# Optimization experiments

Measured on AMD Instinct MI355X. Metric: run time of the kernel, lower is better.

## Reference

```python
import jax, jax.numpy as jnp
import numpy as np

MUL0, MUL1, MUL2, NMOD = 128, 64, 32, 2  # multiplicities of 0e,1e,2e and modalities
D0, D1, D2 = MUL0, MUL1 * 3, MUL2 * 5     # 128, 192, 160 -> total 480


def setup_inputs() -> dict:
    key = jax.random.key(0)
    ks = jax.random.split(key, 7)
    N, G = 200000, 512
    x = jax.random.normal(ks[0], (N, D0 + D1 + D2), dtype=jnp.float32)
    modal_attr = jax.random.uniform(ks[1], (G, NMOD), dtype=jnp.float32)
    W0 = jax.random.normal(ks[2], (MUL0, MUL0), dtype=jnp.float32)
    W0m = jax.random.normal(ks[3], (NMOD, MUL0), dtype=jnp.float32)
    W1 = jax.random.normal(ks[4], (MUL1, MUL1), dtype=jnp.float32)
    W2 = jax.random.normal(ks[5], (MUL2, MUL2), dtype=jnp.float32)
    batch = jnp.sort(jax.random.randint(ks[6], (N,), 0, G, dtype=jnp.int64))
    return {"x": x, "modal_attr": modal_attr, "W0": W0, "W0m": W0m,
            "W1": W1, "W2": W2, "batch": batch}


def reference(x, modal_attr, W0, W0m, W1, W2, batch):
    N = x.shape[0]
    # modality one-hot gathered per node and concatenated (appended 2x0e irrep)
    modal = modal_attr[batch]  # [N, NMOD]
    x0 = x[:, :D0]                                   # [N, 128]  0e
    x1 = x[:, D0:D0 + D1].reshape(N, MUL1, 3)        # [N, 64, 3] 1e
    x2 = x[:, D0 + D1:].reshape(N, MUL2, 5)          # [N, 32, 5] 2e
    # e3nn Linear: per-(l,p) block linear, paths summed, /sqrt(total fan-in mul)
    inv0 = 1.0 / np.sqrt(MUL0 + NMOD).astype(np.float32)
    out0 = (x0 @ W0 + modal @ W0m) * inv0            # [N, 128]
    out1 = jnp.einsum('nim,io->nom', x1, W1) * (1.0 / np.sqrt(MUL1).astype(np.float32))
    out2 = jnp.einsum('nim,io->nom', x2, W2) * (1.0 / np.sqrt(MUL2).astype(np.float32))
    return jnp.concatenate([out0, out1.reshape(N, D1), out2.reshape(N, D2)], axis=1)
```

## Files before the change

### kernel.cpp

```cpp
#include <hip/hip_runtime.h>
#include <hip/hip_bf16.h>


typedef __attribute__((ext_vector_type(8))) short  short8;
typedef __attribute__((ext_vector_type(4))) float  f32x4;

#define NTH 256
#define BR  32

#define W0H 0
#define W0L 16384
#define W1H 32768
#define W1L 36864
#define W2H 40960
#define W2L 41984

#define IN0   0
#define OUT0  24576

__device__ __forceinline__ unsigned bc2(__hip_bfloat162 h) {
    unsigned u; __builtin_memcpy(&u, &h, 4); return u;
}

struct HL4 { uint2 h, l; };

__device__ __forceinline__ HL4 split4(float a, float b, float c, float d) {
    __hip_bfloat162 h01 = __float22bfloat162_rn({a, b});
    __hip_bfloat162 h23 = __float22bfloat162_rn({c, d});
    float ra = a - __low2float(h01),  rb = b - __high2float(h01);
    float rc = c - __low2float(h23),  rd = d - __high2float(h23);
    __hip_bfloat162 l01 = __float22bfloat162_rn({ra, rb});
    __hip_bfloat162 l23 = __float22bfloat162_rn({rc, rd});
    HL4 r;
    r.h = make_uint2(bc2(h01), bc2(h23));
    r.l = make_uint2(bc2(l01), bc2(l23));
    return r;
}

__device__ __forceinline__ void split_w(float v, unsigned short& h, unsigned short& l) {
    __hip_bfloat16 hb = __float2bfloat16(v);
    float r = v - __bfloat162float(hb);
    __hip_bfloat16 lb = __float2bfloat16(r);
    __builtin_memcpy(&h, &hb, 2);
    __builtin_memcpy(&l, &lb, 2);
}

__global__ void prep_weights(const float* __restrict__ W0,
                             const float* __restrict__ W1,
                             const float* __restrict__ W2,
                             unsigned short* __restrict__ ws) {
    const int s0     = blockIdx.x * blockDim.x + threadIdx.x;
    const int STRIDE = gridDim.x * blockDim.x;
    for (int s = s0; s < 16384; s += STRIDE) {
        int j = s & 7, l = (s >> 3) & 63, kt = (s >> 9) & 3, ct = s >> 11;
        int col = ct * 16 + (l & 15);
        int k   = kt * 32 + (l >> 4) * 8 + j;
        unsigned short h, lo;
        split_w(W0[k * 128 + col], h, lo);
        ws[W0H + s] = h; ws[W0L + s] = lo;
    }
    for (int s = s0; s < 4096; s += STRIDE) {
        int j = s & 7, l = (s >> 3) & 63, kt = (s >> 9) & 1, ct = s >> 10;
        int col = ct * 16 + (l & 15);
        int k   = kt * 32 + (l >> 4) * 8 + j;
        unsigned short h, lo;
        split_w(W1[k * 64 + col], h, lo);
        ws[W1H + s] = h; ws[W1L + s] = lo;
    }
    for (int s = s0; s < 1024; s += STRIDE) {
        int j = s & 7, l = (s >> 3) & 63, ct = s >> 9;
        int col = ct * 16 + (l & 15);
        int k   = (l >> 4) * 8 + j;
        unsigned short h, lo;
        split_w(W2[k * 32 + col], h, lo);
        ws[W2H + s] = h; ws[W2L + s] = lo;
    }
}

#define MFMA(a, b, c) __builtin_amdgcn_mfma_f32_16x16x32_bf16((a), (b), (c), 0, 0, 0)

__global__ __launch_bounds__(NTH, 3) void irreps_mfma_kernel(
    const float* __restrict__ x,
    const float* __restrict__ modal_attr,
    const float* __restrict__ W0m,
    const unsigned short* __restrict__ wsf,
    const int*   __restrict__ batch,
    float*       __restrict__ out,
    int N)
{
    __shared__ __align__(16) char ldsb[49664];
    char*  inb  = ldsb + IN0;
    float* ldsf = reinterpret_cast<float*>(ldsb + OUT0);

    const int tid  = threadIdx.x;
    const int w    = tid >> 6;
    const int l    = tid & 63;
    const int r    = l & 15;
    const int kg   = l >> 4;
    const int rb0  = (w >> 1) * 16;
    const int ch   = w & 1;
    const int row0 = blockIdx.x * BR;
    const int arow = rb0 + r;

    float am0[4], am1[4];
    #pragma unroll
    for (int reg = 0; reg < 4; ++reg) {
        int n  = row0 + rb0 + kg * 4 + reg;
        int nc = n < N ? n : N - 1;
        int g  = batch[nc];
        am0[reg] = modal_attr[2 * g];
        am1[reg] = modal_attr[2 * g + 1];
    }

    const float4* __restrict__ x4 = reinterpret_cast<const float4*>(x);

    {
        const int seg = tid & 15;
        const int rr0 = tid >> 4;
        #pragma unroll
        for (int t2 = 0; t2 < 2; ++t2) {
            int rr = rr0 + 16 * t2;
            int n  = row0 + rr; n = n < N ? n : N - 1;
            const float4* src = &x4[(size_t)n * 120 + seg * 2];
            float4 a = src[0], b = src[1];
            HL4 p = split4(a.x, a.y, a.z, a.w);
            HL4 q = split4(b.x, b.y, b.z, b.w);
            int byte = (rr * 256 + seg * 16) ^ ((rr & 7) << 4);
            *reinterpret_cast<uint4*>(inb + byte)        = make_uint4(p.h.x, p.h.y, q.h.x, q.h.y);
            *reinterpret_cast<uint4*>(inb + 8192 + byte) = make_uint4(p.l.x, p.l.y, q.l.x, q.l.y);
        }
    }

    float4 bld[2][3];
    {
        const int ig  = tid & 15;
        const int rr0 = tid >> 4;
        #pragma unroll
        for (int t2 = 0; t2 < 2; ++t2) {
            int rr = rr0 + 16 * t2;
            int n  = row0 + rr; n = n < N ? n : N - 1;
            const float4* src = &x4[(size_t)n * 120 + 32 + ig * 3];
            bld[t2][0] = src[0]; bld[t2][1] = src[1]; bld[t2][2] = src[2];
        }
    }
    __syncthreads();

    {
        const int sw = (arow & 7) << 4;
        short8 ah[4], al[4];
        #pragma unroll
        for (int kt = 0; kt < 4; ++kt) {
            int byte = (arow * 256 + kt * 64 + kg * 16) ^ sw;
            ah[kt] = *reinterpret_cast<const short8*>(inb + byte);
            al[kt] = *reinterpret_cast<const short8*>(inb + 8192 + byte);
        }
        #pragma unroll
        for (int ci = 0; ci < 4; ++ci) {
            int ct = ch * 4 + ci;
            f32x4 acc = {0.f, 0.f, 0.f, 0.f};
            #pragma unroll
            for (int kt = 0; kt < 4; ++kt) {
                int b = ct * 4 + kt;
                short8 bh = *reinterpret_cast<const short8*>(wsf + W0H + (size_t)(b * 64 + l) * 8);
                short8 bl = *reinterpret_cast<const short8*>(wsf + W0L + (size_t)(b * 64 + l) * 8);
                acc = MFMA(ah[kt], bh, acc);
                acc = MFMA(al[kt], bh, acc);
                acc = MFMA(ah[kt], bl, acc);
            }
            int col = ct * 16 + r;
            float wm0 = W0m[col], wm1 = W0m[128 + col];
            #pragma unroll
            for (int reg = 0; reg < 4; ++reg)
                ldsf[(rb0 + kg * 4 + reg) * 132 + col] =
                    (acc[reg] + am0[reg] * wm0 + am1[reg] * wm1) * 0.08770580193070293f;
        }
    }
    __syncthreads();

    {
        const int ig  = tid & 15;
        const int rr0 = tid >> 4;
        #pragma unroll
        for (int t2 = 0; t2 < 2; ++t2) {
            int rr = rr0 + 16 * t2;
            float4 f0 = bld[t2][0], f1 = bld[t2][1], f2 = bld[t2][2];
            HL4 s0 = split4(f0.x, f0.w, f1.z, f2.y);
            HL4 s1 = split4(f0.y, f1.x, f1.w, f2.z);
            HL4 s2 = split4(f0.z, f1.y, f2.x, f2.w);
            int rbyte = (rr * 128 + ig * 8) ^ ((rr & 7) << 4);
            *reinterpret_cast<uint2*>(inb + 0 * 4096 + rbyte)         = s0.h;
            *reinterpret_cast<uint2*>(inb + 1 * 4096 + rbyte)         = s1.h;
            *reinterpret_cast<uint2*>(inb + 2 * 4096 + rbyte)         = s2.h;
            *reinterpret_cast<uint2*>(inb + 12288 + 0 * 4096 + rbyte) = s0.l;
            *reinterpret_cast<uint2*>(inb + 12288 + 1 * 4096 + rbyte) = s1.l;
            *reinterpret_cast<uint2*>(inb + 12288 + 2 * 4096 + rbyte) = s2.l;
        }
    }
    float4 cld[5];
    {
        int rr = tid >> 3, ig = tid & 7;
        int n  = row0 + rr; n = n < N ? n : N - 1;
        const float4* src = &x4[(size_t)n * 120 + 80 + ig * 5];
        #pragma unroll
        for (int q = 0; q < 5; ++q) cld[q] = src[q];
    }
    {
        #pragma unroll
        for (int j = 0; j < 4; ++j) {
            int idx = tid + j * NTH;
            int row = idx >> 5, c4 = idx & 31;
            int n   = row0 + row;
            if (n < N)
                *reinterpret_cast<float4*>(out + (size_t)n * 480 + c4 * 4) =
                    *reinterpret_cast<const float4*>(ldsf + row * 132 + c4 * 4);
        }
    }
    __syncthreads();

    {
        const int sw = (arow & 7) << 4;
        short8 ah1[3][2], al1[3][2];
        #pragma unroll
        for (int m = 0; m < 3; ++m) {
            #pragma unroll
            for (int kt = 0; kt < 2; ++kt) {
                int byte = (arow * 128 + kt * 64 + kg * 16) ^ sw;
                ah1[m][kt] = *reinterpret_cast<const short8*>(inb + m * 4096 + byte);
                al1[m][kt] = *reinterpret_cast<const short8*>(inb + 12288 + m * 4096 + byte);
            }
        }
        #pragma unroll
        for (int ci = 0; ci < 2; ++ci) {
            int ct = ch * 2 + ci;
            short8 bh[2], bl[2];
            #pragma unroll
            for (int kt = 0; kt < 2; ++kt) {
                int b = ct * 2 + kt;
                bh[kt] = *reinterpret_cast<const short8*>(wsf + W1H + (size_t)(b * 64 + l) * 8);
                bl[kt] = *reinterpret_cast<const short8*>(wsf + W1L + (size_t)(b * 64 + l) * 8);
            }
            #pragma unroll
            for (int m = 0; m < 3; ++m) {
                f32x4 acc = {0.f, 0.f, 0.f, 0.f};
                #pragma unroll
                for (int kt = 0; kt < 2; ++kt) {
                    acc = MFMA(ah1[m][kt], bh[kt], acc);
                    acc = MFMA(al1[m][kt], bh[kt], acc);
                    acc = MFMA(ah1[m][kt], bl[kt], acc);
                }
                int col = 3 * (ct * 16 + r) + m;
                #pragma unroll
                for (int reg = 0; reg < 4; ++reg)
                    ldsf[(rb0 + kg * 4 + reg) * 196 + col] = acc[reg] * 0.125f;
            }
        }
    }
    __syncthreads();

    {
        int rr = tid >> 3, ig = tid & 7;
        float f[20];
        #pragma unroll
        for (int q = 0; q < 5; ++q) {
            float4 v = cld[q];
            f[q * 4 + 0] = v.x; f[q * 4 + 1] = v.y; f[q * 4 + 2] = v.z; f[q * 4 + 3] = v.w;
        }
        int rbyte = (rr * 64 + ig * 8) ^ ((rr & 3) << 4);
        #pragma unroll
        for (int m = 0; m < 5; ++m) {
            HL4 s = split4(f[m], f[5 + m], f[10 + m], f[15 + m]);
            *reinterpret_cast<uint2*>(inb + m * 2048 + rbyte)         = s.h;
            *reinterpret_cast<uint2*>(inb + 10240 + m * 2048 + rbyte) = s.l;
        }
    }
    {
        #pragma unroll
        for (int j = 0; j < 6; ++j) {
            int idx = tid + j * NTH;
            int row = idx / 48, c4 = idx - row * 48;
            int n   = row0 + row;
            if (n < N)
                *reinterpret_cast<float4*>(out + (size_t)n * 480 + 128 + c4 * 4) =
                    *reinterpret_cast<const float4*>(ldsf + row * 196 + c4 * 4);
        }
    }
    __syncthreads();

    {
        const int sw2 = (arow & 3) << 4;
        short8 ah2[5], al2[5];
        #pragma unroll
        for (int m = 0; m < 5; ++m) {
            int byte = (arow * 64 + kg * 16) ^ sw2;
            ah2[m] = *reinterpret_cast<const short8*>(inb + m * 2048 + byte);
            al2[m] = *reinterpret_cast<const short8*>(inb + 10240 + m * 2048 + byte);
        }
        int ct = ch;
        short8 bh = *reinterpret_cast<const short8*>(wsf + W2H + (size_t)(ct * 64 + l) * 8);
        short8 bl = *reinterpret_cast<const short8*>(wsf + W2L + (size_t)(ct * 64 + l) * 8);
        #pragma unroll
        for (int m = 0; m < 5; ++m) {
            f32x4 acc = {0.f, 0.f, 0.f, 0.f};
            acc = MFMA(ah2[m], bh, acc);
            acc = MFMA(al2[m], bh, acc);
            acc = MFMA(ah2[m], bl, acc);
            int col = 5 * (ct * 16 + r) + m;
            #pragma unroll
            for (int reg = 0; reg < 4; ++reg)
                ldsf[(rb0 + kg * 4 + reg) * 164 + col] = acc[reg] * 0.17677669529663687f;
        }
    }
    __syncthreads();

    {
        #pragma unroll
        for (int j = 0; j < 5; ++j) {
            int idx = tid + j * NTH;
            int row = idx / 40, c4 = idx - row * 40;
            int n   = row0 + row;
            if (n < N)
                *reinterpret_cast<float4*>(out + (size_t)n * 480 + 320 + c4 * 4) =
                    *reinterpret_cast<const float4*>(ldsf + row * 164 + c4 * 4);
        }
    }
}

extern "C" void kernel_launch(void* const* d_in, const int* in_sizes, int n_in,
                              void* d_out, int out_size, void* d_ws, size_t ws_size,
                              hipStream_t stream) {
    const float* x     = (const float*)d_in[0];
    const float* modal = (const float*)d_in[1];
    const float* W0    = (const float*)d_in[2];
    const float* W0m   = (const float*)d_in[3];
    const float* W1    = (const float*)d_in[4];
    const float* W2    = (const float*)d_in[5];
    const int*   batch = (const int*)d_in[6];
    float* out = (float*)d_out;
    unsigned short* ws = (unsigned short*)d_ws;

    const int N    = in_sizes[6];
    const int grid = (N + BR - 1) / BR;

    prep_weights<<<84, NTH, 0, stream>>>(W0, W1, W2, ws);
    irreps_mfma_kernel<<<grid, NTH, 0, stream>>>(x, modal, W0m, ws, batch, out, N);
}
```

Before: 159.5 us.

## Swap MFMA operands to write outputs directly from registers, dropping LDS staging

MFMA operands are swapped so the weights become the A operand and node rows the B operand. Each lane then holds four consecutive output columns for a single row and can write float4 directly to global memory, with no round-trip through an LDS output buffer. This drops the output staging region, cuts LDS to 24 KB and raises the launch-bounds occupancy target from 3 to 4. The stores are now per-row float4 writes spread over 16 rows per wave, which may coalesce less well than the previous contiguous row copies. The modal lookup is also reduced to one row per lane.

```diff
diff --git a/kernel.cpp b/kernel.cpp
--- a/kernel.cpp
+++ b/kernel.cpp
@@ -14,9 +14,6 @@
 #define W1L 36864
 #define W2H 40960
 #define W2L 41984
-
-#define IN0   0
-#define OUT0  24576
 
 __device__ __forceinline__ unsigned bc2(__hip_bfloat162 h) {
     unsigned u; __builtin_memcpy(&u, &h, 4); return u;
@@ -79,7 +76,7 @@
 
 #define MFMA(a, b, c) __builtin_amdgcn_mfma_f32_16x16x32_bf16((a), (b), (c), 0, 0, 0)
 
-__global__ __launch_bounds__(NTH, 3) void irreps_mfma_kernel(
+__global__ __launch_bounds__(NTH, 4) void irreps_mfma_kernel(
     const float* __restrict__ x,
     const float* __restrict__ modal_attr,
     const float* __restrict__ W0m,
@@ -88,9 +85,7 @@
     float*       __restrict__ out,
     int N)
 {
-    __shared__ __align__(16) char ldsb[49664];
-    char*  inb  = ldsb + IN0;
-    float* ldsf = reinterpret_cast<float*>(ldsb + OUT0);
+    __shared__ __align__(16) char inb[24576];
 
     const int tid  = threadIdx.x;
     const int w    = tid >> 6;
@@ -102,15 +97,13 @@
     const int row0 = blockIdx.x * BR;
     const int arow = rb0 + r;
 
-    float am0[4], am1[4];
-    #pragma unroll
-    for (int reg = 0; reg < 4; ++reg) {
-        int n  = row0 + rb0 + kg * 4 + reg;
-        int nc = n < N ? n : N - 1;
-        int g  = batch[nc];
-        am0[reg] = modal_attr[2 * g];
-        am1[reg] = modal_attr[2 * g + 1];
-    }
+    const int  n_mine = row0 + arow;
+    const bool ok     = n_mine < N;
+    const int  nc     = ok ? n_mine : N - 1;
+    const int  g      = batch[nc];
+    const float m0 = modal_attr[2 * g];
+    const float m1 = modal_attr[2 * g + 1];
+    float* __restrict__ orow = out + (size_t)n_mine * 480;
 
     const float4* __restrict__ x4 = reinterpret_cast<const float4*>(x);
 
@@ -145,34 +138,14 @@
     }
     __syncthreads();
 
+    short8 xh[4], xl[4];
     {
         const int sw = (arow & 7) << 4;
-        short8 ah[4], al[4];
         #pragma unroll
         for (int kt = 0; kt < 4; ++kt) {
             int byte = (arow * 256 + kt * 64 + kg * 16) ^ sw;
-            ah[kt] = *reinterpret_cast<const short8*>(inb + byte);
-            al[kt] = *reinterpret_cast<const short8*>(inb + 8192 + byte);
-        }
-        #pragma unroll
-        for (int ci = 0; ci < 4; ++ci) {
-            int ct = ch * 4 + ci;
-            f32x4 acc = {0.f, 0.f, 0.f, 0.f};
-            #pragma unroll
-            for (int kt = 0; kt < 4; ++kt) {
-                int b = ct * 4 + kt;
-                short8 bh = *reinterpret_cast<const short8*>(wsf + W0H + (size_t)(b * 64 + l) * 8);
-                short8 bl = *reinterpret_cast<const short8*>(wsf + W0L + (size_t)(b * 64 + l) * 8);
-                acc = MFMA(ah[kt], bh, acc);
-                acc = MFMA(al[kt], bh, acc);
-                acc = MFMA(ah[kt], bl, acc);
-            }
-            int col = ct * 16 + r;
-            float wm0 = W0m[col], wm1 = W0m[128 + col];
-            #pragma unroll
-            for (int reg = 0; reg < 4; ++reg)
-                ldsf[(rb0 + kg * 4 + reg) * 132 + col] =
-                    (acc[reg] + am0[reg] * wm0 + am1[reg] * wm1) * 0.08770580193070293f;
+            xh[kt] = *reinterpret_cast<const short8*>(inb + byte);
+            xl[kt] = *reinterpret_cast<const short8*>(inb + 8192 + byte);
         }
     }
     __syncthreads();
@@ -206,121 +179,132 @@
     }
     {
         #pragma unroll
-        for (int j = 0; j < 4; ++j) {
-            int idx = tid + j * NTH;
-            int row = idx >> 5, c4 = idx & 31;
-            int n   = row0 + row;
-            if (n < N)
-                *reinterpret_cast<float4*>(out + (size_t)n * 480 + c4 * 4) =
-                    *reinterpret_cast<const float4*>(ldsf + row * 132 + c4 * 4);
-        }
-    }
-    __syncthreads();
-
+        for (int ci = 0; ci < 4; ++ci) {
+            int ct = ch * 4 + ci;
+            f32x4 acc = {0.f, 0.f, 0.f, 0.f};
+            #pragma unroll
+            for (int kt = 0; kt < 4; ++kt) {
+                int b = ct * 4 + kt;
+                short8 wh = *reinterpret_cast<const short8*>(wsf + W0H + (size_t)(b * 64 + l) * 8);
+                short8 wl = *reinterpret_cast<const short8*>(wsf + W0L + (size_t)(b * 64 + l) * 8);
+                acc = MFMA(wh, xh[kt], acc);
+                acc = MFMA(wh, xl[kt], acc);
+                acc = MFMA(wl, xh[kt], acc);
+            }
+            int col0 = ct * 16 + kg * 4;
+            float4 wm0 = *reinterpret_cast<const float4*>(W0m + col0);
+            float4 wm1 = *reinterpret_cast<const float4*>(W0m + 128 + col0);
+            const float inv0 = 0.08770580193070293f;
+            float4 o;
+            o.x = (acc[0] + m0 * wm0.x + m1 * wm1.x) * inv0;
+            o.y = (acc[1] + m0 * wm0.y + m1 * wm1.y) * inv0;
+            o.z = (acc[2] + m0 * wm0.z + m1 * wm1.z) * inv0;
+            o.w = (acc[3] + m0 * wm0.w + m1 * wm1.w) * inv0;
+            if (ok) *reinterpret_cast<float4*>(orow + col0) = o;
+        }
+    }
+    __syncthreads();
+
+    short8 xh1[3][2], xl1[3][2];
     {
         const int sw = (arow & 7) << 4;
-        short8 ah1[3][2], al1[3][2];
         #pragma unroll
         for (int m = 0; m < 3; ++m) {
             #pragma unroll
             for (int kt = 0; kt < 2; ++kt) {
                 int byte = (arow * 128 + kt * 64 + kg * 16) ^ sw;
-                ah1[m][kt] = *reinterpret_cast<const short8*>(inb + m * 4096 + byte);
-                al1[m][kt] = *reinterpret_cast<const short8*>(inb + 12288 + m * 4096 + byte);
+                xh1[m][kt] = *reinterpret_cast<const short8*>(inb + m * 4096 + byte);
+                xl1[m][kt] = *reinterpret_cast<const short8*>(inb + 12288 + m * 4096 + byte);
             }
         }
+    }
+    __syncthreads();
+
+    {
+        int rr = tid >> 3, ig = tid & 7;
+        float f[20];
+        #pragma unroll
+        for (int q = 0; q < 5; ++q) {
+            float4 v = cld[q];
+            f[q * 4 + 0] = v.x; f[q * 4 + 1] = v.y; f[q * 4 + 2] = v.z; f[q * 4 + 3] = v.w;
+        }
+        int rbyte = (rr * 64 + ig * 8) ^ ((rr & 3) << 4);
+        #pragma unroll
+        for (int m = 0; m < 5; ++m) {
+            HL4 s = split4(f[m], f[5 + m], f[10 + m], f[15 + m]);
+            *reinterpret_cast<uint2*>(inb + m * 2048 + rbyte)         = s.h;
+            *reinterpret_cast<uint2*>(inb + 10240 + m * 2048 + rbyte) = s.l;
+        }
+    }
+    {
+        const float inv1 = 0.125f;
         #pragma unroll
         for (int ci = 0; ci < 2; ++ci) {
             int ct = ch * 2 + ci;
-            short8 bh[2], bl[2];
-            #pragma unroll
-            for (int kt = 0; kt < 2; ++kt) {
-                int b = ct * 2 + kt;
-                bh[kt] = *reinterpret_cast<const short8*>(wsf + W1H + (size_t)(b * 64 + l) * 8);
-                bl[kt] = *reinterpret_cast<const short8*>(wsf + W1L + (size_t)(b * 64 + l) * 8);
-            }
+            f32x4 am[3];
             #pragma unroll
             for (int m = 0; m < 3; ++m) {
                 f32x4 acc = {0.f, 0.f, 0.f, 0.f};
                 #pragma unroll
                 for (int kt = 0; kt < 2; ++kt) {
-                    acc = MFMA(ah1[m][kt], bh[kt], acc);
-                    acc = MFMA(al1[m][kt], bh[kt], acc);
-                    acc = MFMA(ah1[m][kt], bl[kt], acc);
+                    int b = ct * 2 + kt;
+                    short8 wh = *reinterpret_cast<const short8*>(wsf + W1H + (size_t)(b * 64 + l) * 8);
+                    short8 wl = *reinterpret_cast<const short8*>(wsf + W1L + (size_t)(b * 64 + l) * 8);
+                    acc = MFMA(wh, xh1[m][kt], acc);
+                    acc = MFMA(wh, xl1[m][kt], acc);
+                    acc = MFMA(wl, xh1[m][kt], acc);
                 }
-                int col = 3 * (ct * 16 + r) + m;
-                #pragma unroll
-                for (int reg = 0; reg < 4; ++reg)
-                    ldsf[(rb0 + kg * 4 + reg) * 196 + col] = acc[reg] * 0.125f;
+                am[m] = acc;
             }
-        }
-    }
-    __syncthreads();
-
-    {
-        int rr = tid >> 3, ig = tid & 7;
-        float f[20];
-        #pragma unroll
-        for (int q = 0; q < 5; ++q) {
-            float4 v = cld[q];
-            f[q * 4 + 0] = v.x; f[q * 4 + 1] = v.y; f[q * 4 + 2] = v.z; f[q * 4 + 3] = v.w;
-        }
-        int rbyte = (rr * 64 + ig * 8) ^ ((rr & 3) << 4);
-        #pragma unroll
-        for (int m = 0; m < 5; ++m) {
-            HL4 s = split4(f[m], f[5 + m], f[10 + m], f[15 + m]);
-            *reinterpret_cast<uint2*>(inb + m * 2048 + rbyte)         = s.h;
-            *reinterpret_cast<uint2*>(inb + 10240 + m * 2048 + rbyte) = s.l;
-        }
-    }
-    {
-        #pragma unroll
-        for (int j = 0; j < 6; ++j) {
-            int idx = tid + j * NTH;
-            int row = idx / 48, c4 = idx - row * 48;
-            int n   = row0 + row;
-            if (n < N)
-                *reinterpret_cast<float4*>(out + (size_t)n * 480 + 128 + c4 * 4) =
-                    *reinterpret_cast<const float4*>(ldsf + row * 196 + c4 * 4);
+            int oc0 = ct * 16 + kg * 4;
+            float* p = orow + 128 + 3 * oc0;
+            if (ok) {
+                *reinterpret_cast<float4*>(p) =
+                    make_float4(am[0][0] * inv1, am[1][0] * inv1, am[2][0] * inv1, am[0][1] * inv1);
+                *reinterpret_cast<float4*>(p + 4) =
+                    make_float4(am[1][1] * inv1, am[2][1] * inv1, am[0][2] * inv1, am[1][2] * inv1);
+                *reinterpret_cast<float4*>(p + 8) =
+                    make_float4(am[2][2] * inv1, am[0][3] * inv1, am[1][3] * inv1, am[2][3] * inv1);
+            }
         }
     }
     __syncthreads();
 
     {
         const int sw2 = (arow & 3) << 4;
-        short8 ah2[5], al2[5];
+        short8 xh2[5], xl2[5];
         #pragma unroll
         for (int m = 0; m < 5; ++m) {
             int byte = (arow * 64 + kg * 16) ^ sw2;
-            ah2[m] = *reinterpret_cast<const short8*>(inb + m * 2048 + byte);
-            al2[m] = *reinterpret_cast<const short8*>(inb + 10240 + m * 2048 + byte);
+            xh2[m] = *reinterpret_cast<const short8*>(inb + m * 2048 + byte);
+            xl2[m] = *reinterpret_cast<const short8*>(inb + 10240 + m * 2048 + byte);
         }
         int ct = ch;
-        short8 bh = *reinterpret_cast<const short8*>(wsf + W2H + (size_t)(ct * 64 + l) * 8);
-        short8 bl = *reinterpret_cast<const short8*>(wsf + W2L + (size_t)(ct * 64 + l) * 8);
+        short8 wh = *reinterpret_cast<const short8*>(wsf + W2H + (size_t)(ct * 64 + l) * 8);
+        short8 wl = *reinterpret_cast<const short8*>(wsf + W2L + (size_t)(ct * 64 + l) * 8);
+        f32x4 am[5];
         #pragma unroll
         for (int m = 0; m < 5; ++m) {
             f32x4 acc = {0.f, 0.f, 0.f, 0.f};
-            acc = MFMA(ah2[m], bh, acc);
-            acc = MFMA(al2[m], bh, acc);
-            acc = MFMA(ah2[m], bl, acc);
-            int col = 5 * (ct * 16 + r) + m;
-            #pragma unroll
-            for (int reg = 0; reg < 4; ++reg)
-                ldsf[(rb0 + kg * 4 + reg) * 164 + col] = acc[reg] * 0.17677669529663687f;
-        }
-    }
-    __syncthreads();
-
-    {
-        #pragma unroll
-        for (int j = 0; j < 5; ++j) {
-            int idx = tid + j * NTH;
-            int row = idx / 40, c4 = idx - row * 40;
-            int n   = row0 + row;
-            if (n < N)
-                *reinterpret_cast<float4*>(out + (size_t)n * 480 + 320 + c4 * 4) =
-                    *reinterpret_cast<const float4*>(ldsf + row * 164 + c4 * 4);
+            acc = MFMA(wh, xh2[m], acc);
+            acc = MFMA(wh, xl2[m], acc);
+            acc = MFMA(wl, xh2[m], acc);
+            am[m] = acc;
+        }
+        const float inv2 = 0.17677669529663687f;
+        int oc0 = ct * 16 + kg * 4;
+        float* p = orow + 320 + 5 * oc0;
+        if (ok) {
+            *reinterpret_cast<float4*>(p) =
+                make_float4(am[0][0] * inv2, am[1][0] * inv2, am[2][0] * inv2, am[3][0] * inv2);
+            *reinterpret_cast<float4*>(p + 4) =
+                make_float4(am[4][0] * inv2, am[0][1] * inv2, am[1][1] * inv2, am[2][1] * inv2);
+            *reinterpret_cast<float4*>(p + 8) =
+                make_float4(am[3][1] * inv2, am[4][1] * inv2, am[0][2] * inv2, am[1][2] * inv2);
+            *reinterpret_cast<float4*>(p + 12) =
+                make_float4(am[2][2] * inv2, am[3][2] * inv2, am[4][2] * inv2, am[0][3] * inv2);
+            *reinterpret_cast<float4*>(p + 16) =
+                make_float4(am[1][3] * inv2, am[2][3] * inv2, am[3][3] * inv2, am[4][3] * inv2);
         }
     }
 }
```

New measurement: 205.4 us. 28.7% more time.

## Make irreps kernel persistent with cross-tile prefetch of next tile's inputs

Applied to the files above, without the earlier changes.

Launches a fixed grid of 768 blocks that loop over 32-row tiles in a grid-stride fashion instead of one block per tile. Inside the loop, the next tile's 0e and 1e input slices are loaded into registers during the current tile's later stages, so their global-load latency overlaps with MFMA work and output stores. This removes per-block launch and prologue costs, but it adds register pressure from the prefetch buffers and ties occupancy to a fixed grid size. With 768 blocks at 3 blocks per CU, the grid may underfill or imbalance the CUs.

```diff
diff --git a/kernel.cpp b/kernel.cpp
--- a/kernel.cpp
+++ b/kernel.cpp
@@ -7,6 +7,7 @@
 
 #define NTH 256
 #define BR  32
+#define NB  768
 
 #define W0H 0
 #define W0L 16384
@@ -14,9 +15,6 @@
 #define W1L 36864
 #define W2H 40960
 #define W2L 41984
-
-#define IN0   0
-#define OUT0  24576
 
 __device__ __forceinline__ unsigned bc2(__hip_bfloat162 h) {
     unsigned u; __builtin_memcpy(&u, &h, 4); return u;
@@ -89,8 +87,8 @@
     int N)
 {
     __shared__ __align__(16) char ldsb[49664];
-    char*  inb  = ldsb + IN0;
-    float* ldsf = reinterpret_cast<float*>(ldsb + OUT0);
+    char*  inb  = ldsb;
+    float* ldsf = reinterpret_cast<float*>(ldsb + 24576);
 
     const int tid  = threadIdx.x;
     const int w    = tid >> 6;
@@ -99,228 +97,266 @@
     const int kg   = l >> 4;
     const int rb0  = (w >> 1) * 16;
     const int ch   = w & 1;
-    const int row0 = blockIdx.x * BR;
     const int arow = rb0 + r;
-
-    float am0[4], am1[4];
-    #pragma unroll
-    for (int reg = 0; reg < 4; ++reg) {
-        int n  = row0 + rb0 + kg * 4 + reg;
-        int nc = n < N ? n : N - 1;
-        int g  = batch[nc];
-        am0[reg] = modal_attr[2 * g];
-        am1[reg] = modal_attr[2 * g + 1];
-    }
+    const int NT   = (N + BR - 1) / BR;
 
     const float4* __restrict__ x4 = reinterpret_cast<const float4*>(x);
 
+    const int segA = tid & 15, rr0A = tid >> 4;
+    const int igB  = tid & 15, rr0B = tid >> 4;
+    const int rrC  = tid >> 3, igC  = tid & 7;
+
+    int t = blockIdx.x;
+    if (t >= NT) return;
+
     {
-        const int seg = tid & 15;
-        const int rr0 = tid >> 4;
+        const int row0 = t * BR;
         #pragma unroll
         for (int t2 = 0; t2 < 2; ++t2) {
-            int rr = rr0 + 16 * t2;
+            int rr = rr0A + 16 * t2;
             int n  = row0 + rr; n = n < N ? n : N - 1;
-            const float4* src = &x4[(size_t)n * 120 + seg * 2];
+            const float4* src = &x4[(size_t)n * 120 + segA * 2];
             float4 a = src[0], b = src[1];
             HL4 p = split4(a.x, a.y, a.z, a.w);
             HL4 q = split4(b.x, b.y, b.z, b.w);
-            int byte = (rr * 256 + seg * 16) ^ ((rr & 7) << 4);
+            int byte = (rr * 256 + segA * 16) ^ ((rr & 7) << 4);
             *reinterpret_cast<uint4*>(inb + byte)        = make_uint4(p.h.x, p.h.y, q.h.x, q.h.y);
             *reinterpret_cast<uint4*>(inb + 8192 + byte) = make_uint4(p.l.x, p.l.y, q.l.x, q.l.y);
         }
     }
-
     float4 bld[2][3];
     {
-        const int ig  = tid & 15;
-        const int rr0 = tid >> 4;
+        const int row0 = t * BR;
         #pragma unroll
         for (int t2 = 0; t2 < 2; ++t2) {
-            int rr = rr0 + 16 * t2;
+            int rr = rr0B + 16 * t2;
             int n  = row0 + rr; n = n < N ? n : N - 1;
-            const float4* src = &x4[(size_t)n * 120 + 32 + ig * 3];
+            const float4* src = &x4[(size_t)n * 120 + 32 + igB * 3];
             bld[t2][0] = src[0]; bld[t2][1] = src[1]; bld[t2][2] = src[2];
         }
     }
-    __syncthreads();
-
-    {
-        const int sw = (arow & 7) << 4;
-        short8 ah[4], al[4];
+
+    for (; t < NT; t += NB) {
+        const int row0  = t * BR;
+        const int tn    = (t + NB < NT) ? (t + NB) : t;
+        const int nrow0 = tn * BR;
+
+        float am0[4], am1[4];
         #pragma unroll
-        for (int kt = 0; kt < 4; ++kt) {
-            int byte = (arow * 256 + kt * 64 + kg * 16) ^ sw;
-            ah[kt] = *reinterpret_cast<const short8*>(inb + byte);
-            al[kt] = *reinterpret_cast<const short8*>(inb + 8192 + byte);
-        }
-        #pragma unroll
-        for (int ci = 0; ci < 4; ++ci) {
-            int ct = ch * 4 + ci;
-            f32x4 acc = {0.f, 0.f, 0.f, 0.f};
+        for (int reg = 0; reg < 4; ++reg) {
+            int n  = row0 + rb0 + kg * 4 + reg;
+            int nc = n < N ? n : N - 1;
+            int g  = batch[nc];
+            am0[reg] = modal_attr[2 * g];
+            am1[reg] = modal_attr[2 * g + 1];
+        }
+
+        __syncthreads();
+
+        {
+            const int sw = (arow & 7) << 4;
+            short8 ah[4], al[4];
             #pragma unroll
             for (int kt = 0; kt < 4; ++kt) {
-                int b = ct * 4 + kt;
-                short8 bh = *reinterpret_cast<const short8*>(wsf + W0H + (size_t)(b * 64 + l) * 8);
-                short8 bl = *reinterpret_cast<const short8*>(wsf + W0L + (size_t)(b * 64 + l) * 8);
-                acc = MFMA(ah[kt], bh, acc);
-                acc = MFMA(al[kt], bh, acc);
-                acc = MFMA(ah[kt], bl, acc);
-            }
-            int col = ct * 16 + r;
-            float wm0 = W0m[col], wm1 = W0m[128 + col];
-            #pragma unroll
-            for (int reg = 0; reg < 4; ++reg)
-                ldsf[(rb0 + kg * 4 + reg) * 132 + col] =
-                    (acc[reg] + am0[reg] * wm0 + am1[reg] * wm1) * 0.08770580193070293f;
-        }
-    }
-    __syncthreads();
-
-    {
-        const int ig  = tid & 15;
-        const int rr0 = tid >> 4;
-        #pragma unroll
-        for (int t2 = 0; t2 < 2; ++t2) {
-            int rr = rr0 + 16 * t2;
-            float4 f0 = bld[t2][0], f1 = bld[t2][1], f2 = bld[t2][2];
-            HL4 s0 = split4(f0.x, f0.w, f1.z, f2.y);
-            HL4 s1 = split4(f0.y, f1.x, f1.w, f2.z);
-            HL4 s2 = split4(f0.z, f1.y, f2.x, f2.w);
-            int rbyte = (rr * 128 + ig * 8) ^ ((rr & 7) << 4);
-            *reinterpret_cast<uint2*>(inb + 0 * 4096 + rbyte)         = s0.h;
-            *reinterpret_cast<uint2*>(inb + 1 * 4096 + rbyte)         = s1.h;
-            *reinterpret_cast<uint2*>(inb + 2 * 4096 + rbyte)         = s2.h;
-            *reinterpret_cast<uint2*>(inb + 12288 + 0 * 4096 + rbyte) = s0.l;
-            *reinterpret_cast<uint2*>(inb + 12288 + 1 * 4096 + rbyte) = s1.l;
-            *reinterpret_cast<uint2*>(inb + 12288 + 2 * 4096 + rbyte) = s2.l;
-        }
-    }
-    float4 cld[5];
-    {
-        int rr = tid >> 3, ig = tid & 7;
-        int n  = row0 + rr; n = n < N ? n : N - 1;
-        const float4* src = &x4[(size_t)n * 120 + 80 + ig * 5];
-        #pragma unroll
-        for (int q = 0; q < 5; ++q) cld[q] = src[q];
-    }
-    {
-        #pragma unroll
-        for (int j = 0; j < 4; ++j) {
-            int idx = tid + j * NTH;
-            int row = idx >> 5, c4 = idx & 31;
-            int n   = row0 + row;
-            if (n < N)
-                *reinterpret_cast<float4*>(out + (size_t)n * 480 + c4 * 4) =
-                    *reinterpret_cast<const float4*>(ldsf + row * 132 + c4 * 4);
-        }
-    }
-    __syncthreads();
-
-    {
-        const int sw = (arow & 7) << 4;
-        short8 ah1[3][2], al1[3][2];
-        #pragma unroll
-        for (int m = 0; m < 3; ++m) {
-            #pragma unroll
-            for (int kt = 0; kt < 2; ++kt) {
-                int byte = (arow * 128 + kt * 64 + kg * 16) ^ sw;
-                ah1[m][kt] = *reinterpret_cast<const short8*>(inb + m * 4096 + byte);
-                al1[m][kt] = *reinterpret_cast<const short8*>(inb + 12288 + m * 4096 + byte);
-            }
-        }
-        #pragma unroll
-        for (int ci = 0; ci < 2; ++ci) {
-            int ct = ch * 2 + ci;
-            short8 bh[2], bl[2];
-            #pragma unroll
-            for (int kt = 0; kt < 2; ++kt) {
-                int b = ct * 2 + kt;
-                bh[kt] = *reinterpret_cast<const short8*>(wsf + W1H + (size_t)(b * 64 + l) * 8);
-                bl[kt] = *reinterpret_cast<const short8*>(wsf + W1L + (size_t)(b * 64 + l) * 8);
-            }
+                int byte = (arow * 256 + kt * 64 + kg * 16) ^ sw;
+                ah[kt] = *reinterpret_cast<const short8*>(inb + byte);
+                al[kt] = *reinterpret_cast<const short8*>(inb + 8192 + byte);
+            }
+            #pragma unroll
+            for (int ci = 0; ci < 4; ++ci) {
+                int ct = ch * 4 + ci;
+                f32x4 acc = {0.f, 0.f, 0.f, 0.f};
+                #pragma unroll
+                for (int kt = 0; kt < 4; ++kt) {
+                    int b = ct * 4 + kt;
+                    short8 bh = *reinterpret_cast<const short8*>(wsf + W0H + (size_t)(b * 64 + l) * 8);
+                    short8 bl = *reinterpret_cast<const short8*>(wsf + W0L + (size_t)(b * 64 + l) * 8);
+                    acc = MFMA(ah[kt], bh, acc);
+                    acc = MFMA(al[kt], bh, acc);
+                    acc = MFMA(ah[kt], bl, acc);
+                }
+                int col = ct * 16 + r;
+                float wm0 = W0m[col], wm1 = W0m[128 + col];
+                #pragma unroll
+                for (int reg = 0; reg < 4; ++reg)
+                    ldsf[(rb0 + kg * 4 + reg) * 132 + col] =
+                        (acc[reg] + am0[reg] * wm0 + am1[reg] * wm1) * 0.08770580193070293f;
+            }
+        }
+        __syncthreads();
+
+        float4 cld[5];
+        {
+            int n = row0 + rrC; n = n < N ? n : N - 1;
+            const float4* src = &x4[(size_t)n * 120 + 80 + igC * 5];
+            #pragma unroll
+            for (int q = 0; q < 5; ++q) cld[q] = src[q];
+        }
+        {
+            #pragma unroll
+            for (int t2 = 0; t2 < 2; ++t2) {
+                int rr = rr0B + 16 * t2;
+                float4 f0 = bld[t2][0], f1 = bld[t2][1], f2 = bld[t2][2];
+                HL4 s0 = split4(f0.x, f0.w, f1.z, f2.y);
+                HL4 s1 = split4(f0.y, f1.x, f1.w, f2.z);
+                HL4 s2 = split4(f0.z, f1.y, f2.x, f2.w);
+                int rbyte = (rr * 128 + igB * 8) ^ ((rr & 7) << 4);
+                *reinterpret_cast<uint2*>(inb + 0 * 4096 + rbyte)         = s0.h;
+                *reinterpret_cast<uint2*>(inb + 1 * 4096 + rbyte)         = s1.h;
+                *reinterpret_cast<uint2*>(inb + 2 * 4096 + rbyte)         = s2.h;
+                *reinterpret_cast<uint2*>(inb + 12288 + 0 * 4096 + rbyte) = s0.l;
+                *reinterpret_cast<uint2*>(inb + 12288 + 1 * 4096 + rbyte) = s1.l;
+                *reinterpret_cast<uint2*>(inb + 12288 + 2 * 4096 + rbyte) = s2.l;
+            }
+        }
+        {
+            #pragma unroll
+            for (int j = 0; j < 4; ++j) {
+                int idx = tid + j * NTH;
+                int row = idx >> 5, c4 = idx & 31;
+                int n   = row0 + row;
+                if (n < N)
+                    *reinterpret_cast<float4*>(out + (size_t)n * 480 + c4 * 4) =
+                        *reinterpret_cast<const float4*>(ldsf + row * 132 + c4 * 4);
+            }
+        }
+        __syncthreads();
+
+        {
+            const int sw = (arow & 7) << 4;
+            short8 ah1[3][2], al1[3][2];
             #pragma unroll
             for (int m = 0; m < 3; ++m) {
+                #pragma unroll
+                for (int kt = 0; kt < 2; ++kt) {
+                    int byte = (arow * 128 + kt * 64 + kg * 16) ^ sw;
+                    ah1[m][kt] = *reinterpret_cast<const short8*>(inb + m * 4096 + byte);
+                    al1[m][kt] = *reinterpret_cast<const short8*>(inb + 12288 + m * 4096 + byte);
+                }
+            }
+            #pragma unroll
+            for (int ci = 0; ci < 2; ++ci) {
+                int ct = ch * 2 + ci;
+                short8 bh[2], bl[2];
+                #pragma unroll
+                for (int kt = 0; kt < 2; ++kt) {
+                    int b = ct * 2 + kt;
+                    bh[kt] = *reinterpret_cast<const short8*>(wsf + W1H + (size_t)(b * 64 + l) * 8);
+                    bl[kt] = *reinterpret_cast<const short8*>(wsf + W1L + (size_t)(b * 64 + l) * 8);
+                }
+                #pragma unroll
+                for (int m = 0; m < 3; ++m) {
+                    f32x4 acc = {0.f, 0.f, 0.f, 0.f};
+                    #pragma unroll
+                    for (int kt = 0; kt < 2; ++kt) {
+                        acc = MFMA(ah1[m][kt], bh[kt], acc);
+                        acc = MFMA(al1[m][kt], bh[kt], acc);
+                        acc = MFMA(ah1[m][kt], bl[kt], acc);
+                    }
+                    int col = 3 * (ct * 16 + r) + m;
+                    #pragma unroll
+                    for (int reg = 0; reg < 4; ++reg)
+                        ldsf[(rb0 + kg * 4 + reg) * 196 + col] = acc[reg] * 0.125f;
+                }
+            }
+        }
+        __syncthreads();
+
+        {
+            float f[20];
+            #pragma unroll
+            for (int q = 0; q < 5; ++q) {
+                float4 v = cld[q];
+                f[q * 4 + 0] = v.x; f[q * 4 + 1] = v.y; f[q * 4 + 2] = v.z; f[q * 4 + 3] = v.w;
+            }
+            int rbyte = (rrC * 64 + igC * 8) ^ ((rrC & 3) << 4);
+            #pragma unroll
+            for (int m = 0; m < 5; ++m) {
+                HL4 s = split4(f[m], f[5 + m], f[10 + m], f[15 + m]);
+                *reinterpret_cast<uint2*>(inb + m * 2048 + rbyte)         = s.h;
+                *reinterpret_cast<uint2*>(inb + 10240 + m * 2048 + rbyte) = s.l;
+            }
+        }
+        {
+            #pragma unroll
+            for (int j = 0; j < 6; ++j) {
+                int idx = tid + j * NTH;
+                int row = idx / 48, c4 = idx - row * 48;
+                int n   = row0 + row;
+                if (n < N)
+                    *reinterpret_cast<float4*>(out + (size_t)n * 480 + 128 + c4 * 4) =
+                        *reinterpret_cast<const float4*>(ldsf + row * 196 + c4 * 4);
+            }
+        }
+        __syncthreads();
+
+        float4 ald[2][2];
+        {
+            #pragma unroll
+            for (int t2 = 0; t2 < 2; ++t2) {
+                int rr = rr0A + 16 * t2;
+                int n  = nrow0 + rr; n = n < N ? n : N - 1;
+                const float4* src = &x4[(size_t)n * 120 + segA * 2];
+                ald[t2][0] = src[0]; ald[t2][1] = src[1];
+            }
+        }
+        {
+            const int sw2 = (arow & 3) << 4;
+            short8 ah2[5], al2[5];
+            #pragma unroll
+            for (int m = 0; m < 5; ++m) {
+                int byte = (arow * 64 + kg * 16) ^ sw2;
+                ah2[m] = *reinterpret_cast<const short8*>(inb + m * 2048 + byte);
+                al2[m] = *reinterpret_cast<const short8*>(inb + 10240 + m * 2048 + byte);
+            }
+            int ct = ch;
+            short8 bh = *reinterpret_cast<const short8*>(wsf + W2H + (size_t)(ct * 64 + l) * 8);
+            short8 bl = *reinterpret_cast<const short8*>(wsf + W2L + (size_t)(ct * 64 + l) * 8);
+            #pragma unroll
+            for (int m = 0; m < 5; ++m) {
                 f32x4 acc = {0.f, 0.f, 0.f, 0.f};
-                #pragma unroll
-                for (int kt = 0; kt < 2; ++kt) {
-                    acc = MFMA(ah1[m][kt], bh[kt], acc);
-                    acc = MFMA(al1[m][kt], bh[kt], acc);
-                    acc = MFMA(ah1[m][kt], bl[kt], acc);
-                }
-                int col = 3 * (ct * 16 + r) + m;
+                acc = MFMA(ah2[m], bh, acc);
+                acc = MFMA(al2[m], bh, acc);
+                acc = MFMA(ah2[m], bl, acc);
+                int col = 5 * (ct * 16 + r) + m;
                 #pragma unroll
                 for (int reg = 0; reg < 4; ++reg)
-                    ldsf[(rb0 + kg * 4 + reg) * 196 + col] = acc[reg] * 0.125f;
-            }
-        }
-    }
-    __syncthreads();
-
-    {
-        int rr = tid >> 3, ig = tid & 7;
-        float f[20];
-        #pragma unroll
-        for (int q = 0; q < 5; ++q) {
-            float4 v = cld[q];
-            f[q * 4 + 0] = v.x; f[q * 4 + 1] = v.y; f[q * 4 + 2] = v.z; f[q * 4 + 3] = v.w;
-        }
-        int rbyte = (rr * 64 + ig * 8) ^ ((rr & 3) << 4);
-        #pragma unroll
-        for (int m = 0; m < 5; ++m) {
-            HL4 s = split4(f[m], f[5 + m], f[10 + m], f[15 + m]);
-            *reinterpret_cast<uint2*>(inb + m * 2048 + rbyte)         = s.h;
-            *reinterpret_cast<uint2*>(inb + 10240 + m * 2048 + rbyte) = s.l;
-        }
-    }
-    {
-        #pragma unroll
-        for (int j = 0; j < 6; ++j) {
-            int idx = tid + j * NTH;
-            int row = idx / 48, c4 = idx - row * 48;
-            int n   = row0 + row;
-            if (n < N)
-                *reinterpret_cast<float4*>(out + (size_t)n * 480 + 128 + c4 * 4) =
-                    *reinterpret_cast<const float4*>(ldsf + row * 196 + c4 * 4);
-        }
-    }
-    __syncthreads();
-
-    {
-        const int sw2 = (arow & 3) << 4;
-        short8 ah2[5], al2[5];
-        #pragma unroll
-        for (int m = 0; m < 5; ++m) {
-            int byte = (arow * 64 + kg * 16) ^ sw2;
-            ah2[m] = *reinterpret_cast<const short8*>(inb + m * 2048 + byte);
-            al2[m] = *reinterpret_cast<const short8*>(inb + 10240 + m * 2048 + byte);
-        }
-        int ct = ch;
-        short8 bh = *reinterpret_cast<const short8*>(wsf + W2H + (size_t)(ct * 64 + l) * 8);
-        short8 bl = *reinterpret_cast<const short8*>(wsf + W2L + (size_t)(ct * 64 + l) * 8);
-        #pragma unroll
-        for (int m = 0; m < 5; ++m) {
-            f32x4 acc = {0.f, 0.f, 0.f, 0.f};
-            acc = MFMA(ah2[m], bh, acc);
-            acc = MFMA(al2[m], bh, acc);
-            acc = MFMA(ah2[m], bl, acc);
-            int col = 5 * (ct * 16 + r) + m;
-            #pragma unroll
-            for (int reg = 0; reg < 4; ++reg)
-                ldsf[(rb0 + kg * 4 + reg) * 164 + col] = acc[reg] * 0.17677669529663687f;
-        }
-    }
-    __syncthreads();
-
-    {
-        #pragma unroll
-        for (int j = 0; j < 5; ++j) {
-            int idx = tid + j * NTH;
-            int row = idx / 40, c4 = idx - row * 40;
-            int n   = row0 + row;
-            if (n < N)
-                *reinterpret_cast<float4*>(out + (size_t)n * 480 + 320 + c4 * 4) =
-                    *reinterpret_cast<const float4*>(ldsf + row * 164 + c4 * 4);
+                    ldsf[(rb0 + kg * 4 + reg) * 164 + col] = acc[reg] * 0.17677669529663687f;
+            }
+        }
+        __syncthreads();
+
+        {
+            #pragma unroll
+            for (int t2 = 0; t2 < 2; ++t2) {
+                int rr = rr0A + 16 * t2;
+                float4 a = ald[t2][0], b = ald[t2][1];
+                HL4 p = split4(a.x, a.y, a.z, a.w);
+                HL4 q = split4(b.x, b.y, b.z, b.w);
+                int byte = (rr * 256 + segA * 16) ^ ((rr & 7) << 4);
+                *reinterpret_cast<uint4*>(inb + byte)        = make_uint4(p.h.x, p.h.y, q.h.x, q.h.y);
+                *reinterpret_cast<uint4*>(inb + 8192 + byte) = make_uint4(p.l.x, p.l.y, q.l.x, q.l.y);
+            }
+        }
+        {
+            #pragma unroll
+            for (int t2 = 0; t2 < 2; ++t2) {
+                int rr = rr0B + 16 * t2;
+                int n  = nrow0 + rr; n = n < N ? n : N - 1;
+                const float4* src = &x4[(size_t)n * 120 + 32 + igB * 3];
+                bld[t2][0] = src[0]; bld[t2][1] = src[1]; bld[t2][2] = src[2];
+            }
+        }
+        {
+            #pragma unroll
+            for (int j = 0; j < 5; ++j) {
+                int idx = tid + j * NTH;
+                int row = idx / 40, c4 = idx - row * 40;
+                int n   = row0 + row;
+                if (n < N)
+                    *reinterpret_cast<float4*>(out + (size_t)n * 480 + 320 + c4 * 4) =
+                        *reinterpret_cast<const float4*>(ldsf + row * 164 + c4 * 4);
+            }
         }
     }
 }
@@ -338,8 +374,9 @@
     float* out = (float*)d_out;
     unsigned short* ws = (unsigned short*)d_ws;
 
-    const int N    = in_sizes[6];
-    const int grid = (N + BR - 1) / BR;
+    const int N  = in_sizes[6];
+    const int NT = (N + BR - 1) / BR;
+    const int grid = NT < NB ? NT : NB;
 
     prep_weights<<<84, NTH, 0, stream>>>(W0, W1, W2, ws);
     irreps_mfma_kernel<<<grid, NTH, 0, stream>>>(x, modal, W0m, ws, batch, out, N);
```

After: 351.1 us. +120.1%, slower.

## Double block to 512 threads, splitting output column tiles across eight waves

Applied to the files above, without the earlier changes.

Raises the block from 256 to 512 threads while keeping 32 rows per block, so each wave handles fewer output column tiles in every stage. The W2 stage's five m-slices are split 3/2 across wave pairs. The block-1 LDS repack is moved after the first barrier and merged with the out0 store, which removes one barrier. This gives more waves per CU to hide memory latency, at the cost of more redundant weight fragment loads and some idle threads in the W2 part.

```diff
diff --git a/kernel.cpp b/kernel.cpp
--- a/kernel.cpp
+++ b/kernel.cpp
@@ -5,7 +5,7 @@
 typedef __attribute__((ext_vector_type(8))) short  short8;
 typedef __attribute__((ext_vector_type(4))) float  f32x4;
 
-#define NTH 256
+#define NTH 512
 #define BR  32
 
 #define W0H 0
@@ -14,9 +14,6 @@
 #define W1L 36864
 #define W2H 40960
 #define W2L 41984
-
-#define IN0   0
-#define OUT0  24576
 
 __device__ __forceinline__ unsigned bc2(__hip_bfloat162 h) {
     unsigned u; __builtin_memcpy(&u, &h, 4); return u;
@@ -79,7 +76,7 @@
 
 #define MFMA(a, b, c) __builtin_amdgcn_mfma_f32_16x16x32_bf16((a), (b), (c), 0, 0, 0)
 
-__global__ __launch_bounds__(NTH, 3) void irreps_mfma_kernel(
+__global__ __launch_bounds__(NTH, 4) void irreps_mfma_kernel(
     const float* __restrict__ x,
     const float* __restrict__ modal_attr,
     const float* __restrict__ W0m,
@@ -89,16 +86,16 @@
     int N)
 {
     __shared__ __align__(16) char ldsb[49664];
-    char*  inb  = ldsb + IN0;
-    float* ldsf = reinterpret_cast<float*>(ldsb + OUT0);
+    char*  inb  = ldsb;
+    float* ldsf = reinterpret_cast<float*>(ldsb + 24576);
 
     const int tid  = threadIdx.x;
     const int w    = tid >> 6;
     const int l    = tid & 63;
     const int r    = l & 15;
     const int kg   = l >> 4;
-    const int rb0  = (w >> 1) * 16;
-    const int ch   = w & 1;
+    const int rb0  = (w >> 2) * 16;
+    const int ch   = w & 3;
     const int row0 = blockIdx.x * BR;
     const int arow = rb0 + r;
 
@@ -116,32 +113,24 @@
 
     {
         const int seg = tid & 15;
-        const int rr0 = tid >> 4;
-        #pragma unroll
-        for (int t2 = 0; t2 < 2; ++t2) {
-            int rr = rr0 + 16 * t2;
-            int n  = row0 + rr; n = n < N ? n : N - 1;
-            const float4* src = &x4[(size_t)n * 120 + seg * 2];
-            float4 a = src[0], b = src[1];
-            HL4 p = split4(a.x, a.y, a.z, a.w);
-            HL4 q = split4(b.x, b.y, b.z, b.w);
-            int byte = (rr * 256 + seg * 16) ^ ((rr & 7) << 4);
-            *reinterpret_cast<uint4*>(inb + byte)        = make_uint4(p.h.x, p.h.y, q.h.x, q.h.y);
-            *reinterpret_cast<uint4*>(inb + 8192 + byte) = make_uint4(p.l.x, p.l.y, q.l.x, q.l.y);
-        }
-    }
-
-    float4 bld[2][3];
-    {
-        const int ig  = tid & 15;
-        const int rr0 = tid >> 4;
-        #pragma unroll
-        for (int t2 = 0; t2 < 2; ++t2) {
-            int rr = rr0 + 16 * t2;
-            int n  = row0 + rr; n = n < N ? n : N - 1;
-            const float4* src = &x4[(size_t)n * 120 + 32 + ig * 3];
-            bld[t2][0] = src[0]; bld[t2][1] = src[1]; bld[t2][2] = src[2];
-        }
+        const int rr  = tid >> 4;
+        int n = row0 + rr; n = n < N ? n : N - 1;
+        const float4* src = &x4[(size_t)n * 120 + seg * 2];
+        float4 a = src[0], b = src[1];
+        HL4 p = split4(a.x, a.y, a.z, a.w);
+        HL4 q = split4(b.x, b.y, b.z, b.w);
+        int byte = (rr * 256 + seg * 16) ^ ((rr & 7) << 4);
+        *reinterpret_cast<uint4*>(inb + byte)        = make_uint4(p.h.x, p.h.y, q.h.x, q.h.y);
+        *reinterpret_cast<uint4*>(inb + 8192 + byte) = make_uint4(p.l.x, p.l.y, q.l.x, q.l.y);
+    }
+
+    float4 bld[3];
+    {
+        const int ig = tid & 15;
+        const int rr = tid >> 4;
+        int n = row0 + rr; n = n < N ? n : N - 1;
+        const float4* src = &x4[(size_t)n * 120 + 32 + ig * 3];
+        bld[0] = src[0]; bld[1] = src[1]; bld[2] = src[2];
     }
     __syncthreads();
 
@@ -155,8 +144,8 @@
             al[kt] = *reinterpret_cast<const short8*>(inb + 8192 + byte);
         }
         #pragma unroll
-        for (int ci = 0; ci < 4; ++ci) {
-            int ct = ch * 4 + ci;
+        for (int ci = 0; ci < 2; ++ci) {
+            int ct = ch * 2 + ci;
             f32x4 acc = {0.f, 0.f, 0.f, 0.f};
             #pragma unroll
             for (int kt = 0; kt < 4; ++kt) {
@@ -177,27 +166,8 @@
     }
     __syncthreads();
 
-    {
-        const int ig  = tid & 15;
-        const int rr0 = tid >> 4;
-        #pragma unroll
-        for (int t2 = 0; t2 < 2; ++t2) {
-            int rr = rr0 + 16 * t2;
-            float4 f0 = bld[t2][0], f1 = bld[t2][1], f2 = bld[t2][2];
-            HL4 s0 = split4(f0.x, f0.w, f1.z, f2.y);
-            HL4 s1 = split4(f0.y, f1.x, f1.w, f2.z);
-            HL4 s2 = split4(f0.z, f1.y, f2.x, f2.w);
-            int rbyte = (rr * 128 + ig * 8) ^ ((rr & 7) << 4);
-            *reinterpret_cast<uint2*>(inb + 0 * 4096 + rbyte)         = s0.h;
-            *reinterpret_cast<uint2*>(inb + 1 * 4096 + rbyte)         = s1.h;
-            *reinterpret_cast<uint2*>(inb + 2 * 4096 + rbyte)         = s2.h;
-            *reinterpret_cast<uint2*>(inb + 12288 + 0 * 4096 + rbyte) = s0.l;
-            *reinterpret_cast<uint2*>(inb + 12288 + 1 * 4096 + rbyte) = s1.l;
-            *reinterpret_cast<uint2*>(inb + 12288 + 2 * 4096 + rbyte) = s2.l;
-        }
-    }
     float4 cld[5];
-    {
+    if (tid < 256) {
         int rr = tid >> 3, ig = tid & 7;
         int n  = row0 + rr; n = n < N ? n : N - 1;
         const float4* src = &x4[(size_t)n * 120 + 80 + ig * 5];
@@ -205,8 +175,23 @@
         for (int q = 0; q < 5; ++q) cld[q] = src[q];
     }
     {
-        #pragma unroll
-        for (int j = 0; j < 4; ++j) {
+        const int ig = tid & 15;
+        const int rr = tid >> 4;
+        float4 f0 = bld[0], f1 = bld[1], f2 = bld[2];
+        HL4 s0 = split4(f0.x, f0.w, f1.z, f2.y);
+        HL4 s1 = split4(f0.y, f1.x, f1.w, f2.z);
+        HL4 s2 = split4(f0.z, f1.y, f2.x, f2.w);
+        int rbyte = (rr * 128 + ig * 8) ^ ((rr & 7) << 4);
+        *reinterpret_cast<uint2*>(inb + 0 * 4096 + rbyte)         = s0.h;
+        *reinterpret_cast<uint2*>(inb + 1 * 4096 + rbyte)         = s1.h;
+        *reinterpret_cast<uint2*>(inb + 2 * 4096 + rbyte)         = s2.h;
+        *reinterpret_cast<uint2*>(inb + 12288 + 0 * 4096 + rbyte) = s0.l;
+        *reinterpret_cast<uint2*>(inb + 12288 + 1 * 4096 + rbyte) = s1.l;
+        *reinterpret_cast<uint2*>(inb + 12288 + 2 * 4096 + rbyte) = s2.l;
+    }
+    {
+        #pragma unroll
+        for (int j = 0; j < 2; ++j) {
             int idx = tid + j * NTH;
             int row = idx >> 5, c4 = idx & 31;
             int n   = row0 + row;
@@ -229,35 +214,32 @@
                 al1[m][kt] = *reinterpret_cast<const short8*>(inb + 12288 + m * 4096 + byte);
             }
         }
-        #pragma unroll
-        for (int ci = 0; ci < 2; ++ci) {
-            int ct = ch * 2 + ci;
-            short8 bh[2], bl[2];
+        const int ct = ch;
+        short8 bh[2], bl[2];
+        #pragma unroll
+        for (int kt = 0; kt < 2; ++kt) {
+            int b = ct * 2 + kt;
+            bh[kt] = *reinterpret_cast<const short8*>(wsf + W1H + (size_t)(b * 64 + l) * 8);
+            bl[kt] = *reinterpret_cast<const short8*>(wsf + W1L + (size_t)(b * 64 + l) * 8);
+        }
+        #pragma unroll
+        for (int m = 0; m < 3; ++m) {
+            f32x4 acc = {0.f, 0.f, 0.f, 0.f};
             #pragma unroll
             for (int kt = 0; kt < 2; ++kt) {
-                int b = ct * 2 + kt;
-                bh[kt] = *reinterpret_cast<const short8*>(wsf + W1H + (size_t)(b * 64 + l) * 8);
-                bl[kt] = *reinterpret_cast<const short8*>(wsf + W1L + (size_t)(b * 64 + l) * 8);
-            }
-            #pragma unroll
-            for (int m = 0; m < 3; ++m) {
-                f32x4 acc = {0.f, 0.f, 0.f, 0.f};
-                #pragma unroll
-                for (int kt = 0; kt < 2; ++kt) {
-                    acc = MFMA(ah1[m][kt], bh[kt], acc);
-                    acc = MFMA(al1[m][kt], bh[kt], acc);
-                    acc = MFMA(ah1[m][kt], bl[kt], acc);
-                }
-                int col = 3 * (ct * 16 + r) + m;
-                #pragma unroll
-                for (int reg = 0; reg < 4; ++reg)
-                    ldsf[(rb0 + kg * 4 + reg) * 196 + col] = acc[reg] * 0.125f;
-            }
-        }
-    }
-    __syncthreads();
-
-    {
+                acc = MFMA(ah1[m][kt], bh[kt], acc);
+                acc = MFMA(al1[m][kt], bh[kt], acc);
+                acc = MFMA(ah1[m][kt], bl[kt], acc);
+            }
+            int col = 3 * (ct * 16 + r) + m;
+            #pragma unroll
+            for (int reg = 0; reg < 4; ++reg)
+                ldsf[(rb0 + kg * 4 + reg) * 196 + col] = acc[reg] * 0.125f;
+        }
+    }
+    __syncthreads();
+
+    if (tid < 256) {
         int rr = tid >> 3, ig = tid & 7;
         float f[20];
         #pragma unroll
@@ -275,7 +257,7 @@
     }
     {
         #pragma unroll
-        for (int j = 0; j < 6; ++j) {
+        for (int j = 0; j < 3; ++j) {
             int idx = tid + j * NTH;
             int row = idx / 48, c4 = idx - row * 48;
             int n   = row0 + row;
@@ -288,39 +270,42 @@
 
     {
         const int sw2 = (arow & 3) << 4;
-        short8 ah2[5], al2[5];
-        #pragma unroll
-        for (int m = 0; m < 5; ++m) {
-            int byte = (arow * 64 + kg * 16) ^ sw2;
-            ah2[m] = *reinterpret_cast<const short8*>(inb + m * 2048 + byte);
-            al2[m] = *reinterpret_cast<const short8*>(inb + 10240 + m * 2048 + byte);
-        }
-        int ct = ch;
+        const int ct  = ch >> 1;
+        const int mb  = (ch & 1) ? 3 : 0;
+        const int mn  = (ch & 1) ? 2 : 3;
         short8 bh = *reinterpret_cast<const short8*>(wsf + W2H + (size_t)(ct * 64 + l) * 8);
         short8 bl = *reinterpret_cast<const short8*>(wsf + W2L + (size_t)(ct * 64 + l) * 8);
         #pragma unroll
-        for (int m = 0; m < 5; ++m) {
-            f32x4 acc = {0.f, 0.f, 0.f, 0.f};
-            acc = MFMA(ah2[m], bh, acc);
-            acc = MFMA(al2[m], bh, acc);
-            acc = MFMA(ah2[m], bl, acc);
-            int col = 5 * (ct * 16 + r) + m;
-            #pragma unroll
-            for (int reg = 0; reg < 4; ++reg)
-                ldsf[(rb0 + kg * 4 + reg) * 164 + col] = acc[reg] * 0.17677669529663687f;
-        }
-    }
-    __syncthreads();
-
-    {
-        #pragma unroll
-        for (int j = 0; j < 5; ++j) {
+        for (int mm = 0; mm < 3; ++mm) {
+            if (mm < mn) {
+                int m = mb + mm;
+                int byte = (arow * 64 + kg * 16) ^ sw2;
+                short8 ah = *reinterpret_cast<const short8*>(inb + m * 2048 + byte);
+                short8 al = *reinterpret_cast<const short8*>(inb + 10240 + m * 2048 + byte);
+                f32x4 acc = {0.f, 0.f, 0.f, 0.f};
+                acc = MFMA(ah, bh, acc);
+                acc = MFMA(al, bh, acc);
+                acc = MFMA(ah, bl, acc);
+                int col = 5 * (ct * 16 + r) + m;
+                #pragma unroll
+                for (int reg = 0; reg < 4; ++reg)
+                    ldsf[(rb0 + kg * 4 + reg) * 164 + col] = acc[reg] * 0.17677669529663687f;
+            }
+        }
+    }
+    __syncthreads();
+
+    {
+        #pragma unroll
+        for (int j = 0; j < 3; ++j) {
             int idx = tid + j * NTH;
-            int row = idx / 40, c4 = idx - row * 40;
-            int n   = row0 + row;
-            if (n < N)
-                *reinterpret_cast<float4*>(out + (size_t)n * 480 + 320 + c4 * 4) =
-                    *reinterpret_cast<const float4*>(ldsf + row * 164 + c4 * 4);
+            if (idx < 1280) {
+                int row = idx / 40, c4 = idx - row * 40;
+                int n   = row0 + row;
+                if (n < N)
+                    *reinterpret_cast<float4*>(out + (size_t)n * 480 + 320 + c4 * 4) =
+                        *reinterpret_cast<const float4*>(ldsf + row * 164 + c4 * 4);
+            }
         }
     }
 }
@@ -341,6 +326,6 @@
     const int N    = in_sizes[6];
     const int grid = (N + BR - 1) / BR;
 
-    prep_weights<<<84, NTH, 0, stream>>>(W0, W1, W2, ws);
+    prep_weights<<<84, 256, 0, stream>>>(W0, W1, W2, ws);
     irreps_mfma_kernel<<<grid, NTH, 0, stream>>>(x, modal, W0m, ws, batch, out, N);
 }
```

New measurement: 163.4 us. 2.5% more time.
